# Kernel optimization log

Measured on AMD Instinct MI355X. Metric: run time of the kernel, lower is better.

Reference implementation:

```python
import jax, jax.numpy as jnp
import numpy as np

B, NE, NAO, NMO = 1024, 128, 128, 128   # walkers, electrons, AOs, MOs
NC, D = 32, 64                          # n configurations, orbitals per config
MO_SCALE = 0.2 / np.sqrt(NAO)           # keeps 64x64 dets O(1) in fp32


def setup_inputs() -> dict:
    key = jax.random.key(0)
    k1, k2, k3, k4 = jax.random.split(key, 4)
    x = jax.random.normal(k1, (B, NE, NAO), dtype=jnp.float32)
    W_mo = jax.random.normal(k2, (NMO, NAO), dtype=jnp.float32) * MO_SCALE
    W_ci = jax.random.normal(k4, (1, NC), dtype=jnp.float32) / np.sqrt(NC)
    # each config: D distinct sorted orbital indices in [0, NMO)
    configs = jax.vmap(lambda k: jax.random.permutation(k, NMO)[:D])(
        jax.random.split(k3, NC))
    configs = jnp.sort(configs, axis=1).astype(jnp.int32)
    return {"x": x, "W_mo": W_mo, "W_ci": W_ci, "configs": configs}


def reference(x, W_mo, W_ci, configs):
    # layer_mo: [B, NE, NAO] @ [NAO, NMO] -> [B, NE, NMO]
    mo = jnp.einsum('ben,mn->bem', x, W_mo)
    # SlaterPooling, fully batched:
    # sub[b, c, i, j] = mo[b, configs[c, i], configs[c, j]]
    rows = configs[:, :, None]   # [NC, D, 1]
    cols = configs[:, None, :]   # [NC, 1, D]
    sub = mo[:, rows, cols]      # [B, NC, D, D]
    dets = jnp.linalg.det(sub)   # [B, NC]
    # layer_ci: Linear(NC, 1, bias=False)
    return dets @ W_ci.T         # [B, 1]
```

## Files before the change

kernel.cpp:

```cpp
#include <hip/hip_runtime.h>


constexpr int NE  = 128;
constexpr int NAO = 128;
constexpr int D   = 64;

constexpr int MOS = 129;
constexpr int GS  = 132;

constexpr float TAU = 0.02f;

__device__ __forceinline__ float readlane_f(float v, int lane) {
  return __int_as_float(__builtin_amdgcn_readlane(__float_as_int(v), lane));
}

__global__ __launch_bounds__(256) void wavenet_kernel(
    const float* __restrict__ x, const float* __restrict__ W_mo,
    const float* __restrict__ W_ci, const int* __restrict__ configs,
    float* __restrict__ out) {
  __shared__ float mo_ls[128 * MOS];
  __shared__ float x_ls[8 * GS];
  __shared__ float w_ls[8 * GS];
  __shared__ float partial[4];

  const int t    = threadIdx.x;
  const int b    = blockIdx.x;
  const int lane = t & 63;
  const int w    = t >> 6;

  const int tx = t & 15, ty = t >> 4;
  const int c0 = tx * 8, r0 = ty * 8;
  const float* xb = x + (size_t)b * NE * NAO;

  float acc[8][8];
#pragma unroll
  for (int i = 0; i < 8; ++i)
#pragma unroll
    for (int j = 0; j < 8; ++j) acc[i][j] = 0.f;

  const int le = t >> 1;
  const int lh = (t & 1) * 4;

  for (int kb = 0; kb < 16; ++kb) {
    const float4 xv = *reinterpret_cast<const float4*>(xb + le * NAO + kb * 8 + lh);
    const float4 wv = *reinterpret_cast<const float4*>(W_mo + le * NAO + kb * 8 + lh);
    x_ls[(lh + 0) * GS + le] = xv.x;
    x_ls[(lh + 1) * GS + le] = xv.y;
    x_ls[(lh + 2) * GS + le] = xv.z;
    x_ls[(lh + 3) * GS + le] = xv.w;
    w_ls[(lh + 0) * GS + le] = wv.x;
    w_ls[(lh + 1) * GS + le] = wv.y;
    w_ls[(lh + 2) * GS + le] = wv.z;
    w_ls[(lh + 3) * GS + le] = wv.w;
    __syncthreads();
#pragma unroll
    for (int nn = 0; nn < 8; ++nn) {
      const float4 a0 = *reinterpret_cast<const float4*>(&x_ls[nn * GS + r0]);
      const float4 a1 = *reinterpret_cast<const float4*>(&x_ls[nn * GS + r0 + 4]);
      const float4 b0 = *reinterpret_cast<const float4*>(&w_ls[nn * GS + c0]);
      const float4 b1 = *reinterpret_cast<const float4*>(&w_ls[nn * GS + c0 + 4]);
      const float av[8] = {a0.x, a0.y, a0.z, a0.w, a1.x, a1.y, a1.z, a1.w};
      const float bv[8] = {b0.x, b0.y, b0.z, b0.w, b1.x, b1.y, b1.z, b1.w};
#pragma unroll
      for (int i = 0; i < 8; ++i)
#pragma unroll
        for (int j = 0; j < 8; ++j) acc[i][j] = fmaf(av[i], bv[j], acc[i][j]);
    }
    __syncthreads();
  }
#pragma unroll
  for (int i = 0; i < 8; ++i)
#pragma unroll
    for (int j = 0; j < 8; ++j) mo_ls[(r0 + i) * MOS + c0 + j] = acc[i][j];
  __syncthreads();

  float waveacc = 0.f;

#pragma unroll 1
  for (int cc = 0; cc < 8; ++cc) {
    const int c = w * 8 + cc;
    const int cjv     = configs[c * D + lane];
    const int rowbase = cjv * MOS;

    float a[64];
#pragma unroll
    for (int j = 0; j < 64; ++j) {
      const int cj = __builtin_amdgcn_readlane(cjv, j);
      a[j] = mo_ls[rowbase + cj];
    }

    int myslot = lane;
    float det  = 1.f;

#pragma unroll
    for (int k = 0; k < 64; ++k) {
      const float ak  = a[k];
      unsigned long long dbal = __ballot(myslot == k);
      int   p  = (int)__builtin_ctzll(dbal);
      float pv = readlane_f(ak, p);

      if (!(fabsf(pv) > TAU)) {
        const bool act = (myslot >= k);
        unsigned long long cbal = __ballot(act && (fabsf(ak) > TAU));
        if (cbal == 0ull) {
          float v = act ? fabsf(ak) : -1.f;
#pragma unroll
          for (int off = 32; off; off >>= 1) v = fmaxf(v, __shfl_xor(v, off));
          cbal = __ballot(act && (fabsf(ak) == v));
          if (cbal == 0ull) cbal = __ballot(act);
        }
        p  = (int)__builtin_ctzll(cbal);
        pv = readlane_f(ak, p);
        const int sp = __builtin_amdgcn_readlane(myslot, p);
        if (sp != k) det = -det;
        myslot = (lane == p) ? k : ((myslot == k) ? sp : myslot);
      }

      float invp;
      if (pv != 0.f) {
        invp = __builtin_amdgcn_rcpf(pv);
        invp = invp * (2.f - pv * invp);
        det *= pv;
      } else {
        det  = 0.f;
        invp = 0.f;
      }

      const float m = (myslot > k) ? ak * invp : 0.f;
#pragma unroll
      for (int j = k + 1; j < 64; ++j)
        a[j] = fmaf(-m, readlane_f(a[j], p), a[j]);
    }
    waveacc += det * W_ci[c];
  }

  if (lane == 0) partial[w] = waveacc;
  __syncthreads();
  if (t == 0) out[b] = partial[0] + partial[1] + partial[2] + partial[3];
}

extern "C" void kernel_launch(void* const* d_in, const int* in_sizes, int n_in,
                              void* d_out, int out_size, void* d_ws, size_t ws_size,
                              hipStream_t stream) {
  (void)in_sizes; (void)n_in; (void)d_ws; (void)ws_size; (void)out_size;
  const float* x       = (const float*)d_in[0];
  const float* W_mo    = (const float*)d_in[1];
  const float* W_ci    = (const float*)d_in[2];
  const int*   configs = (const int*)d_in[3];
  float*       out     = (float*)d_out;
  hipLaunchKernelGGL(wavenet_kernel, dim3(1024), dim3(256), 0, stream,
                     x, W_mo, W_ci, configs, out);
}
```

Baseline: 538.0 us.

## Double block to 512 threads, alias GEMM staging into MO buffer

```diff
diff --git a/kernel.cpp b/kernel.cpp
--- a/kernel.cpp
+++ b/kernel.cpp
@@ -14,14 +14,16 @@
   return __int_as_float(__builtin_amdgcn_readlane(__float_as_int(v), lane));
 }
 
-__global__ __launch_bounds__(256) void wavenet_kernel(
+__global__ __launch_bounds__(512, 4) void wavenet_kernel(
     const float* __restrict__ x, const float* __restrict__ W_mo,
     const float* __restrict__ W_ci, const int* __restrict__ configs,
     float* __restrict__ out) {
-  __shared__ float mo_ls[128 * MOS];
-  __shared__ float x_ls[8 * GS];
-  __shared__ float w_ls[8 * GS];
-  __shared__ float partial[4];
+  __shared__ float smem[128 * MOS];
+  __shared__ float partial[8];
+
+  float* const mo_ls = smem;
+  float* const x_ls  = smem;
+  float* const w_ls  = smem + 16 * GS;
 
   const int t    = threadIdx.x;
   const int b    = blockIdx.x;
@@ -29,47 +31,47 @@
   const int w    = t >> 6;
 
   const int tx = t & 15, ty = t >> 4;
-  const int c0 = tx * 8, r0 = ty * 8;
+  const int c0 = tx * 8, r0 = ty * 4;
   const float* xb = x + (size_t)b * NE * NAO;
 
-  float acc[8][8];
+  float acc[4][8];
 #pragma unroll
-  for (int i = 0; i < 8; ++i)
+  for (int i = 0; i < 4; ++i)
 #pragma unroll
     for (int j = 0; j < 8; ++j) acc[i][j] = 0.f;
 
-  const int le = t >> 1;
-  const int lh = (t & 1) * 4;
+  const int le = t >> 2;
+  const int lq = (t & 3) * 4;
 
-  for (int kb = 0; kb < 16; ++kb) {
-    const float4 xv = *reinterpret_cast<const float4*>(xb + le * NAO + kb * 8 + lh);
-    const float4 wv = *reinterpret_cast<const float4*>(W_mo + le * NAO + kb * 8 + lh);
-    x_ls[(lh + 0) * GS + le] = xv.x;
-    x_ls[(lh + 1) * GS + le] = xv.y;
-    x_ls[(lh + 2) * GS + le] = xv.z;
-    x_ls[(lh + 3) * GS + le] = xv.w;
-    w_ls[(lh + 0) * GS + le] = wv.x;
-    w_ls[(lh + 1) * GS + le] = wv.y;
-    w_ls[(lh + 2) * GS + le] = wv.z;
-    w_ls[(lh + 3) * GS + le] = wv.w;
+  for (int kb = 0; kb < 8; ++kb) {
+    const float4 xv = *reinterpret_cast<const float4*>(xb + le * NAO + kb * 16 + lq);
+    const float4 wv = *reinterpret_cast<const float4*>(W_mo + le * NAO + kb * 16 + lq);
+    __syncthreads();
+    x_ls[(lq + 0) * GS + le] = xv.x;
+    x_ls[(lq + 1) * GS + le] = xv.y;
+    x_ls[(lq + 2) * GS + le] = xv.z;
+    x_ls[(lq + 3) * GS + le] = xv.w;
+    w_ls[(lq + 0) * GS + le] = wv.x;
+    w_ls[(lq + 1) * GS + le] = wv.y;
+    w_ls[(lq + 2) * GS + le] = wv.z;
+    w_ls[(lq + 3) * GS + le] = wv.w;
     __syncthreads();
 #pragma unroll
-    for (int nn = 0; nn < 8; ++nn) {
-      const float4 a0 = *reinterpret_cast<const float4*>(&x_ls[nn * GS + r0]);
-      const float4 a1 = *reinterpret_cast<const float4*>(&x_ls[nn * GS + r0 + 4]);
-      const float4 b0 = *reinterpret_cast<const float4*>(&w_ls[nn * GS + c0]);
-      const float4 b1 = *reinterpret_cast<const float4*>(&w_ls[nn * GS + c0 + 4]);
-      const float av[8] = {a0.x, a0.y, a0.z, a0.w, a1.x, a1.y, a1.z, a1.w};
-      const float bv[8] = {b0.x, b0.y, b0.z, b0.w, b1.x, b1.y, b1.z, b1.w};
+    for (int kk = 0; kk < 16; ++kk) {
+      const float4 av = *reinterpret_cast<const float4*>(&x_ls[kk * GS + r0]);
+      const float4 b0 = *reinterpret_cast<const float4*>(&w_ls[kk * GS + c0]);
+      const float4 b1 = *reinterpret_cast<const float4*>(&w_ls[kk * GS + c0 + 4]);
+      const float aa[4] = {av.x, av.y, av.z, av.w};
+      const float bb[8] = {b0.x, b0.y, b0.z, b0.w, b1.x, b1.y, b1.z, b1.w};
 #pragma unroll
-      for (int i = 0; i < 8; ++i)
+      for (int i = 0; i < 4; ++i)
 #pragma unroll
-        for (int j = 0; j < 8; ++j) acc[i][j] = fmaf(av[i], bv[j], acc[i][j]);
+        for (int j = 0; j < 8; ++j) acc[i][j] = fmaf(aa[i], bb[j], acc[i][j]);
     }
-    __syncthreads();
   }
+  __syncthreads();
 #pragma unroll
-  for (int i = 0; i < 8; ++i)
+  for (int i = 0; i < 4; ++i)
 #pragma unroll
     for (int j = 0; j < 8; ++j) mo_ls[(r0 + i) * MOS + c0 + j] = acc[i][j];
   __syncthreads();
@@ -77,8 +79,8 @@
   float waveacc = 0.f;
 
 #pragma unroll 1
-  for (int cc = 0; cc < 8; ++cc) {
-    const int c = w * 8 + cc;
+  for (int cc = 0; cc < 4; ++cc) {
+    const int c = w * 4 + cc;
     const int cjv     = configs[c * D + lane];
     const int rowbase = cjv * MOS;
 
@@ -136,7 +138,12 @@
 
   if (lane == 0) partial[w] = waveacc;
   __syncthreads();
-  if (t == 0) out[b] = partial[0] + partial[1] + partial[2] + partial[3];
+  if (t == 0) {
+    float s = 0.f;
+#pragma unroll
+    for (int i = 0; i < 8; ++i) s += partial[i];
+    out[b] = s;
+  }
 }
 
 extern "C" void kernel_launch(void* const* d_in, const int* in_sizes, int n_in,
@@ -148,6 +155,6 @@
   const float* W_ci    = (const float*)d_in[2];
   const int*   configs = (const int*)d_in[3];
   float*       out     = (float*)d_out;
-  hipLaunchKernelGGL(wavenet_kernel, dim3(1024), dim3(256), 0, stream,
+  hipLaunchKernelGGL(wavenet_kernel, dim3(1024), dim3(512), 0, stream,
                      x, W_mo, W_ci, configs, out);
 }
```

Result: no change. 533.5 us (-0.8%).

## Block the LU elimination into panels of eight with LDS-staged trailing updates

Applied to the files above, without the earlier changes.

```diff
diff --git a/kernel.cpp b/kernel.cpp
--- a/kernel.cpp
+++ b/kernel.cpp
@@ -7,6 +7,8 @@
 
 constexpr int MOS = 129;
 constexpr int GS  = 132;
+constexpr int NB  = 8;
+constexpr int UPS = 68;
 
 constexpr float TAU = 0.02f;
 
@@ -18,15 +20,19 @@
     const float* __restrict__ x, const float* __restrict__ W_mo,
     const float* __restrict__ W_ci, const int* __restrict__ configs,
     float* __restrict__ out) {
-  __shared__ float mo_ls[128 * MOS];
-  __shared__ float x_ls[8 * GS];
-  __shared__ float w_ls[8 * GS];
+  __shared__ float smem[16512 + 4 * NB * UPS];
   __shared__ float partial[4];
+
+  float* const mo_ls = smem;
+  float* const x_ls  = smem + 16512;
+  float* const w_ls  = smem + 16512 + 1056;
 
   const int t    = threadIdx.x;
   const int b    = blockIdx.x;
   const int lane = t & 63;
   const int w    = t >> 6;
+
+  float* const up = smem + 16512 + w * (NB * UPS);
 
   const int tx = t & 15, ty = t >> 4;
   const int c0 = tx * 8, r0 = ty * 8;
@@ -93,43 +99,127 @@
     float det  = 1.f;
 
 #pragma unroll
-    for (int k = 0; k < 64; ++k) {
-      const float ak  = a[k];
-      unsigned long long dbal = __ballot(myslot == k);
-      int   p  = (int)__builtin_ctzll(dbal);
-      float pv = readlane_f(ak, p);
-
-      if (!(fabsf(pv) > TAU)) {
-        const bool act = (myslot >= k);
-        unsigned long long cbal = __ballot(act && (fabsf(ak) > TAU));
-        if (cbal == 0ull) {
-          float v = act ? fabsf(ak) : -1.f;
-#pragma unroll
-          for (int off = 32; off; off >>= 1) v = fmaxf(v, __shfl_xor(v, off));
-          cbal = __ballot(act && (fabsf(ak) == v));
-          if (cbal == 0ull) cbal = __ballot(act);
-        }
-        p  = (int)__builtin_ctzll(cbal);
-        pv = readlane_f(ak, p);
-        const int sp = __builtin_amdgcn_readlane(myslot, p);
-        if (sp != k) det = -det;
-        myslot = (lane == p) ? k : ((myslot == k) ? sp : myslot);
+    for (int tB = 0; tB < 8; ++tB) {
+      const int kb  = tB * NB;
+      const int wtr = 64 - (kb + NB);
+
+      float mloc[NB];
+      int   pl[NB];
+
+#pragma unroll
+      for (int i = 0; i < NB; ++i) {
+        const int k = kb + i;
+        const float ak = a[k];
+        unsigned long long dbal = __ballot(myslot == k);
+        int   p  = (int)__builtin_ctzll(dbal);
+        float pv = readlane_f(ak, p);
+
+        if (!(fabsf(pv) > TAU)) {
+          const bool act = (myslot >= k);
+          unsigned long long cbal = __ballot(act && (fabsf(ak) > TAU));
+          if (cbal == 0ull) {
+            float v = act ? fabsf(ak) : -1.f;
+#pragma unroll
+            for (int off = 32; off; off >>= 1) v = fmaxf(v, __shfl_xor(v, off));
+            cbal = __ballot(act && (fabsf(ak) == v));
+            if (cbal == 0ull) cbal = __ballot(act);
+          }
+          p  = (int)__builtin_ctzll(cbal);
+          pv = readlane_f(ak, p);
+          const int sp = __builtin_amdgcn_readlane(myslot, p);
+          if (sp != k) det = -det;
+          myslot = (lane == p) ? k : ((myslot == k) ? sp : myslot);
+        }
+
+        float invp;
+        if (pv != 0.f) {
+          invp = __builtin_amdgcn_rcpf(pv);
+          invp = invp * (2.f - pv * invp);
+          det *= pv;
+        } else {
+          det  = 0.f;
+          invp = 0.f;
+        }
+
+        const float m = (myslot > k) ? ak * invp : 0.f;
+        mloc[i] = m;
+        pl[i]   = p;
+#pragma unroll
+        for (int j = k + 1; j < kb + NB; ++j)
+          a[j] = fmaf(-m, readlane_f(a[j], p), a[j]);
       }
 
-      float invp;
-      if (pv != 0.f) {
-        invp = __builtin_amdgcn_rcpf(pv);
-        invp = invp * (2.f - pv * invp);
-        det *= pv;
-      } else {
-        det  = 0.f;
-        invp = 0.f;
+      if (wtr > 0) {
+        if (myslot >= kb && myslot < kb + NB) {
+          float* dst = up + (myslot - kb) * UPS;
+#pragma unroll
+          for (int j4 = kb + NB; j4 < 64; j4 += 4) {
+            float4 v;
+            v.x = a[j4 + 0]; v.y = a[j4 + 1]; v.z = a[j4 + 2]; v.w = a[j4 + 3];
+            *reinterpret_cast<float4*>(dst + (j4 - kb - NB)) = v;
+          }
+        }
+
+        if (lane < wtr) {
+          float u[NB];
+          float* col = up + lane;
+#pragma unroll
+          for (int tt = 0; tt < NB; ++tt) u[tt] = col[tt * UPS];
+#pragma unroll
+          for (int i = 1; i < NB; ++i) {
+#pragma unroll
+            for (int tt = 0; tt < i; ++tt)
+              u[i] = fmaf(-readlane_f(mloc[tt], pl[i]), u[tt], u[i]);
+          }
+#pragma unroll
+          for (int i = 1; i < NB; ++i) col[i * UPS] = u[i];
+        }
+
+#pragma unroll
+        for (int j4 = kb + NB; j4 < 64; j4 += 4) {
+          const int o = j4 - (kb + NB);
+          const float4 q0 = *reinterpret_cast<const float4*>(up + 0 * UPS + o);
+          const float4 q1 = *reinterpret_cast<const float4*>(up + 1 * UPS + o);
+          const float4 q2 = *reinterpret_cast<const float4*>(up + 2 * UPS + o);
+          const float4 q3 = *reinterpret_cast<const float4*>(up + 3 * UPS + o);
+          const float4 q4 = *reinterpret_cast<const float4*>(up + 4 * UPS + o);
+          const float4 q5 = *reinterpret_cast<const float4*>(up + 5 * UPS + o);
+          const float4 q6 = *reinterpret_cast<const float4*>(up + 6 * UPS + o);
+          const float4 q7 = *reinterpret_cast<const float4*>(up + 7 * UPS + o);
+          a[j4 + 0] = fmaf(-mloc[0], q0.x, a[j4 + 0]);
+          a[j4 + 0] = fmaf(-mloc[1], q1.x, a[j4 + 0]);
+          a[j4 + 0] = fmaf(-mloc[2], q2.x, a[j4 + 0]);
+          a[j4 + 0] = fmaf(-mloc[3], q3.x, a[j4 + 0]);
+          a[j4 + 0] = fmaf(-mloc[4], q4.x, a[j4 + 0]);
+          a[j4 + 0] = fmaf(-mloc[5], q5.x, a[j4 + 0]);
+          a[j4 + 0] = fmaf(-mloc[6], q6.x, a[j4 + 0]);
+          a[j4 + 0] = fmaf(-mloc[7], q7.x, a[j4 + 0]);
+          a[j4 + 1] = fmaf(-mloc[0], q0.y, a[j4 + 1]);
+          a[j4 + 1] = fmaf(-mloc[1], q1.y, a[j4 + 1]);
+          a[j4 + 1] = fmaf(-mloc[2], q2.y, a[j4 + 1]);
+          a[j4 + 1] = fmaf(-mloc[3], q3.y, a[j4 + 1]);
+          a[j4 + 1] = fmaf(-mloc[4], q4.y, a[j4 + 1]);
+          a[j4 + 1] = fmaf(-mloc[5], q5.y, a[j4 + 1]);
+          a[j4 + 1] = fmaf(-mloc[6], q6.y, a[j4 + 1]);
+          a[j4 + 1] = fmaf(-mloc[7], q7.y, a[j4 + 1]);
+          a[j4 + 2] = fmaf(-mloc[0], q0.z, a[j4 + 2]);
+          a[j4 + 2] = fmaf(-mloc[1], q1.z, a[j4 + 2]);
+          a[j4 + 2] = fmaf(-mloc[2], q2.z, a[j4 + 2]);
+          a[j4 + 2] = fmaf(-mloc[3], q3.z, a[j4 + 2]);
+          a[j4 + 2] = fmaf(-mloc[4], q4.z, a[j4 + 2]);
+          a[j4 + 2] = fmaf(-mloc[5], q5.z, a[j4 + 2]);
+          a[j4 + 2] = fmaf(-mloc[6], q6.z, a[j4 + 2]);
+          a[j4 + 2] = fmaf(-mloc[7], q7.z, a[j4 + 2]);
+          a[j4 + 3] = fmaf(-mloc[0], q0.w, a[j4 + 3]);
+          a[j4 + 3] = fmaf(-mloc[1], q1.w, a[j4 + 3]);
+          a[j4 + 3] = fmaf(-mloc[2], q2.w, a[j4 + 3]);
+          a[j4 + 3] = fmaf(-mloc[3], q3.w, a[j4 + 3]);
+          a[j4 + 3] = fmaf(-mloc[4], q4.w, a[j4 + 3]);
+          a[j4 + 3] = fmaf(-mloc[5], q5.w, a[j4 + 3]);
+          a[j4 + 3] = fmaf(-mloc[6], q6.w, a[j4 + 3]);
+          a[j4 + 3] = fmaf(-mloc[7], q7.w, a[j4 + 3]);
+        }
       }
-
-      const float m = (myslot > k) ? ak * invp : 0.f;
-#pragma unroll
-      for (int j = k + 1; j < 64; ++j)
-        a[j] = fmaf(-m, readlane_f(a[j], p), a[j]);
     }
     waveacc += det * W_ci[c];
   }
```

Result: slower. 637.7 us (+18.5%).
